# Performance work log

Measured on AMD Instinct MI355X. Metric: run time of the kernel, lower is better.

Reference implementation:

```python
import jax, jax.numpy as jnp
import numpy as np


def _qkernel(r, i, j, k):
    # Build the real-valued block kernel of a quaternion dense layer.
    # r,i,j,k: [in/4, out/4] -> kernel [in, out] implementing the Hamilton product.
    col_r = jnp.concatenate([r, -i, -j, -k], axis=0)
    col_i = jnp.concatenate([i, r, -k, j], axis=0)
    col_j = jnp.concatenate([j, k, r, -i], axis=0)
    col_k = jnp.concatenate([k, -j, i, r], axis=0)
    return jnp.concatenate([col_r, col_i, col_j, col_k], axis=1)


def setup_inputs() -> dict:
    key = jax.random.key(0)
    ks = jax.random.split(key, 12)
    B, F, H = 32768, 1024, 256
    F4, H4 = F // 4, H // 4
    s_in = 1.0 / np.sqrt(F)
    s_h = 1.0 / np.sqrt(H)
    inp = {
        "x": jax.random.normal(ks[0], (B, F), dtype=jnp.float32),
        "wx_r": jax.random.normal(ks[1], (4, F4, H4), dtype=jnp.float32) * s_in,
        "wx_i": jax.random.normal(ks[2], (4, F4, H4), dtype=jnp.float32) * s_in,
        "wx_j": jax.random.normal(ks[3], (4, F4, H4), dtype=jnp.float32) * s_in,
        "wx_k": jax.random.normal(ks[4], (4, F4, H4), dtype=jnp.float32) * s_in,
        "bx": jnp.zeros((4, H), dtype=jnp.float32),
        "uh_r": jax.random.normal(ks[5], (4, H4, H4), dtype=jnp.float32) * s_h,
        "uh_i": jax.random.normal(ks[6], (4, H4, H4), dtype=jnp.float32) * s_h,
        "uh_j": jax.random.normal(ks[7], (4, H4, H4), dtype=jnp.float32) * s_h,
        "uh_k": jax.random.normal(ks[8], (4, H4, H4), dtype=jnp.float32) * s_h,
        "fco_w": jax.random.normal(ks[9], (H, H), dtype=jnp.float32) * s_h,
        "fco_b": jnp.zeros((H,), dtype=jnp.float32),
    }
    return inp


def reference(x, wx_r, wx_i, wx_j, wx_k, bx, uh_r, uh_i, uh_j, uh_k, fco_w, fco_b):
    # Single-step quaternion LSTM cell with zero initial hidden/cell state.
    # Gate order along leading axis: [forget, input, output, cell].
    Kx = jax.vmap(_qkernel)(wx_r, wx_i, wx_j, wx_k)   # [4, F, H]
    Ku = jax.vmap(_qkernel)(uh_r, uh_i, uh_j, uh_k)   # [4, H, H]
    H = bx.shape[1]
    h0 = jnp.zeros((x.shape[0], H), dtype=x.dtype)
    c0 = h0
    gx = jnp.einsum('bf,gfh->gbh', x, Kx) + bx[:, None, :]   # [4, B, H]
    gu = jnp.einsum('bh,ghk->gbk', h0, Ku)                    # [4, B, H]
    z = gx + gu
    ft = jax.nn.sigmoid(z[0])
    it = jax.nn.sigmoid(z[1])
    ot = jax.nn.sigmoid(z[2])
    at = z[3]
    c = it * jnp.tanh(at) + ft * c0
    h = ot * jnp.tanh(c)
    return h @ fco_w + fco_b
```

## Files before the change

kernel.cpp:

```cpp
#include <hip/hip_runtime.h>
#include <cstdint>
#include <cstddef>

#define WS_WP   0
#define WS_FCO  1572864
#define WS_BP   1703936
#define WS_HVP  1707008

typedef __attribute__((ext_vector_type(8))) __bf16 bf16x8;
typedef __attribute__((ext_vector_type(4))) __bf16 bf16x4;
typedef __attribute__((ext_vector_type(4))) float floatx4;

__device__ __forceinline__ unsigned short f2bf(float f) {
  unsigned int u = __builtin_bit_cast(unsigned int, f);
  u += 0x7fffu + ((u >> 16) & 1u);
  return (unsigned short)(u >> 16);
}

__device__ __forceinline__ float sigmf(float z) {
  return __builtin_amdgcn_rcpf(1.f + __expf(-z));
}
__device__ __forceinline__ float tanh_(float z) {
  return 1.f - 2.f * __builtin_amdgcn_rcpf(1.f + __expf(2.f * z));
}

__device__ __forceinline__ void gld16(const void* g, void* l) {
  __builtin_amdgcn_global_load_lds(
      (const __attribute__((address_space(1))) unsigned int*)g,
      (__attribute__((address_space(3))) unsigned int*)l, 16, 0, 0);
}

__global__ __launch_bounds__(256) void pack_k(
    const float* __restrict__ wr, const float* __restrict__ wi,
    const float* __restrict__ wj, const float* __restrict__ wk,
    const float* __restrict__ bx, const float* __restrict__ fw,
    unsigned short* __restrict__ Wp, unsigned short* __restrict__ Fp,
    float* __restrict__ bp) {
  int t = threadIdx.x;
  if (blockIdx.x < 384) {
    int gpp = blockIdx.x >> 7;
    int oct = blockIdx.x & 127;
    int gp = gpp + 1;
    int h = t;
    int hb = h >> 6, hr = h & 63;
    int f0 = oct << 3;
    int fb = f0 >> 8, fr0 = f0 & 255;
    const int   comp_t[4][4] = {{0,1,2,3},{1,0,3,2},{2,3,0,1},{3,2,1,0}};
    const float sign_t[4][4] = {{1.f,-1.f,-1.f,-1.f},{1.f,1.f,-1.f,1.f},
                                {1.f,1.f,1.f,-1.f},{1.f,-1.f,1.f,1.f}};
    const float* srcs[4] = {wr, wi, wj, wk};
    const float* s = srcs[comp_t[hb][fb]] + ((size_t)((gp << 8) + fr0)) * 64 + hr;
    float sg = sign_t[hb][fb];
    unsigned short v[8];
#pragma unroll
    for (int j = 0; j < 8; ++j) v[j] = f2bf(sg * s[(size_t)j * 64]);
    int c = h * 3 + gpp;
    int cb = c / 192, nl = c % 192;
    int kb = oct >> 2, q = oct & 3;
    int idx16 = (nl << 2) + (q ^ ((nl >> 1) & 3));
    uint4 val = make_uint4(
        (unsigned)v[0] | ((unsigned)v[1] << 16), (unsigned)v[2] | ((unsigned)v[3] << 16),
        (unsigned)v[4] | ((unsigned)v[5] << 16), (unsigned)v[6] | ((unsigned)v[7] << 16));
    *(uint4*)(Wp + (size_t)(cb * 32 + kb) * 6144 + idx16 * 8) = val;
    if (oct == 0) bp[c] = bx[(gp << 8) + h];
  } else {
    int oct = blockIdx.x - 384;
    int n = t;
    int k0 = oct << 3;
    unsigned short v[8];
#pragma unroll
    for (int j = 0; j < 8; ++j) v[j] = f2bf(fw[(size_t)(k0 + j) * 256 + n]);
    int nb = n >> 7, nl = n & 127, kb = oct >> 2, q = oct & 3;
    int idx16 = (nl << 2) + (q ^ ((nl >> 1) & 3));
    uint4 val = make_uint4(
        (unsigned)v[0] | ((unsigned)v[1] << 16), (unsigned)v[2] | ((unsigned)v[3] << 16),
        (unsigned)v[4] | ((unsigned)v[5] << 16), (unsigned)v[6] | ((unsigned)v[7] << 16));
    *(uint4*)(Fp + (size_t)((nb << 3) + kb) * 4096 + idx16 * 8) = val;
  }
}

__global__ __launch_bounds__(256, 2) void gemm1_k(
    const float* __restrict__ x, const unsigned short* __restrict__ Wp,
    const float* __restrict__ bp, unsigned short* __restrict__ hvp) {
  __shared__ char smem[40960];
  float* zep = (float*)smem;

  const int t = threadIdx.x;
  const int lane = t & 63, wid = t >> 6;
  const int wm = wid >> 1, wn = wid & 1;
  const int lrow = lane & 15, q = lane >> 4;
  const int rowt = blockIdx.x;
  const int cby = blockIdx.y;
  const int row0 = rowt * 128;
  const float* xbase = x + (size_t)row0 * 1024;
  const unsigned short* wpb = Wp + (size_t)cby * 32 * 6144;

  const int sr = t >> 3, skq = t & 7;
  const int sq8 = skq >> 1, shalf = skq & 1;

  floatx4 acc[4][6];
#pragma unroll
  for (int i = 0; i < 4; ++i)
#pragma unroll
    for (int j = 0; j < 6; ++j) acc[i][j] = (floatx4){0.f, 0.f, 0.f, 0.f};

#define STAGE_B(buf, kt)                                                      \
  {                                                                           \
    unsigned short* sBs_ = (unsigned short*)(smem + (buf) * 20480 + 8192);    \
    const unsigned short* bt_ = wpb + (size_t)(kt) * 6144;                    \
    _Pragma("unroll")                                                         \
    for (int i_ = 0; i_ < 3; ++i_) {                                          \
      int s_ = t + i_ * 256;                                                  \
      gld16(bt_ + s_ * 8, sBs_ + s_ * 8);                                     \
    }                                                                         \
  }
#define LOAD_A(ra, kt)                                                        \
  {                                                                           \
    const float* ab_ = xbase + (kt) * 32 + skq * 4;                           \
    _Pragma("unroll")                                                         \
    for (int i_ = 0; i_ < 4; ++i_)                                            \
      ra[i_] = *(const float4*)(ab_ + (size_t)(i_ * 32 + sr) * 1024);         \
  }
#define WRITE_A(ra, buf)                                                      \
  {                                                                           \
    unsigned short* sAs_ = (unsigned short*)(smem + (buf) * 20480);           \
    _Pragma("unroll")                                                         \
    for (int i_ = 0; i_ < 4; ++i_) {                                          \
      int m_ = i_ * 32 + sr;                                                  \
      int slot_ = (m_ << 2) + (sq8 ^ ((m_ >> 1) & 3));                        \
      bf16x4 v_;                                                              \
      v_[0] = (__bf16)ra[i_].x; v_[1] = (__bf16)ra[i_].y;                     \
      v_[2] = (__bf16)ra[i_].z; v_[3] = (__bf16)ra[i_].w;                     \
      *(bf16x4*)(sAs_ + slot_ * 8 + shalf * 4) = v_;                          \
    }                                                                         \
  }

  {
    float4 r0[4];
    LOAD_A(r0, 0)
    STAGE_B(0, 0)
    WRITE_A(r0, 0)
  }
  float4 ra[4];
  for (int kt = 0; kt < 32; ++kt) {
    __syncthreads();
    if (kt < 31) {
      LOAD_A(ra, kt + 1)
      STAGE_B((kt + 1) & 1, kt + 1)
    }
    const unsigned short* sA = (const unsigned short*)(smem + (kt & 1) * 20480);
    const unsigned short* sB = sA + 4096;
    bf16x8 af[4], bf[6];
#pragma unroll
    for (int mt = 0; mt < 4; ++mt) {
      int m = wm * 64 + mt * 16 + lrow;
      int slot = (m << 2) + (q ^ ((m >> 1) & 3));
      af[mt] = *(const bf16x8*)(const void*)(sA + slot * 8);
    }
#pragma unroll
    for (int nt = 0; nt < 6; ++nt) {
      int n = wn * 96 + nt * 16 + lrow;
      int off16 = (n << 2) + (q ^ ((n >> 1) & 3));
      bf[nt] = *(const bf16x8*)(const void*)(sB + off16 * 8);
    }
#pragma unroll
    for (int mt = 0; mt < 4; ++mt)
#pragma unroll
      for (int nt = 0; nt < 6; ++nt)
        acc[mt][nt] = __builtin_amdgcn_mfma_f32_16x16x32_bf16(af[mt], bf[nt], acc[mt][nt], 0, 0, 0);
    if (kt < 31) WRITE_A(ra, (kt + 1) & 1)
  }
#undef STAGE_B
#undef LOAD_A
#undef WRITE_A
  __syncthreads();

  const float* bp0 = bp + cby * 192;
  const int er = t >> 3, oc = t & 7;
#pragma unroll
  for (int pass = 0; pass < 4; ++pass) {
    if (wm == (pass >> 1)) {
      int mtb = (pass & 1) * 2;
#pragma unroll
      for (int mi = 0; mi < 2; ++mi)
#pragma unroll
        for (int nt = 0; nt < 6; ++nt)
#pragma unroll
          for (int r = 0; r < 4; ++r)
            zep[(mi * 16 + q * 4 + r) * 201 + wn * 96 + nt * 16 + lrow] = acc[mtb + mi][nt][r];
    }
    __syncthreads();
    {
      int ml = pass * 32 + er;
      unsigned short v[8];
#pragma unroll
      for (int j = 0; j < 8; ++j) {
        int hl = oc * 8 + j;
        float zi = zep[er * 201 + hl * 3 + 0] + bp0[hl * 3 + 0];
        float zo = zep[er * 201 + hl * 3 + 1] + bp0[hl * 3 + 1];
        float zc = zep[er * 201 + hl * 3 + 2] + bp0[hl * 3 + 2];
        float it = sigmf(zi);
        float ot = sigmf(zo);
        float cc = it * tanh_(zc);
        v[j] = f2bf(ot * tanh_(cc));
      }
      int ktile = cby * 2 + (oc >> 2), qq = oc & 3;
      int idx16 = (ml << 2) + (qq ^ ((ml >> 1) & 3));
      uint4 val = make_uint4(
          (unsigned)v[0] | ((unsigned)v[1] << 16), (unsigned)v[2] | ((unsigned)v[3] << 16),
          (unsigned)v[4] | ((unsigned)v[5] << 16), (unsigned)v[6] | ((unsigned)v[7] << 16));
      *(uint4*)(hvp + (size_t)(rowt * 8 + ktile) * 4096 + idx16 * 8) = val;
    }
    __syncthreads();
  }
}

__global__ __launch_bounds__(256, 4) void gemm2_k(
    const unsigned short* __restrict__ hvp, const unsigned short* __restrict__ Fp,
    const float* __restrict__ fcob, float* __restrict__ out) {
  __shared__ unsigned short sB[32768];
  const int t = threadIdx.x;
  const int lane = t & 63, wid = t >> 6;
  const int wm = wid >> 1, wn = wid & 1;
  const int lrow = lane & 15, q = lane >> 4;
  const int mb = blockIdx.x, nb = blockIdx.y;

  const unsigned short* fpb = Fp + (size_t)nb * 32768;
#pragma unroll
  for (int i = 0; i < 16; ++i) gld16(fpb + (t + i * 256) * 8, sB + (t + i * 256) * 8);

  floatx4 acc[4][4];
#pragma unroll
  for (int i = 0; i < 4; ++i)
#pragma unroll
    for (int j = 0; j < 4; ++j) acc[i][j] = (floatx4){0.f, 0.f, 0.f, 0.f};
  __syncthreads();

#pragma unroll
  for (int kt = 0; kt < 8; ++kt) {
    const unsigned short* at_ = hvp + (size_t)(mb * 8 + kt) * 4096;
    bf16x8 af[4], bf[4];
#pragma unroll
    for (int mt = 0; mt < 4; ++mt) {
      int m = wm * 64 + mt * 16 + lrow;
      int o = (m << 2) + (q ^ ((m >> 1) & 3));
      af[mt] = *(const bf16x8*)(const void*)(at_ + o * 8);
    }
#pragma unroll
    for (int nt = 0; nt < 4; ++nt) {
      int n = wn * 64 + nt * 16 + lrow;
      int o = (n << 2) + (q ^ ((n >> 1) & 3));
      bf[nt] = *(const bf16x8*)(const void*)(sB + kt * 4096 + o * 8);
    }
#pragma unroll
    for (int mt = 0; mt < 4; ++mt)
#pragma unroll
      for (int nt = 0; nt < 4; ++nt)
        acc[mt][nt] = __builtin_amdgcn_mfma_f32_16x16x32_bf16(af[mt], bf[nt], acc[mt][nt], 0, 0, 0);
  }
#pragma unroll
  for (int nt = 0; nt < 4; ++nt) {
    int colg = nb * 128 + wn * 64 + nt * 16 + lrow;
    float bias = fcob[colg];
#pragma unroll
    for (int mt = 0; mt < 4; ++mt) {
      int rowg = mb * 128 + wm * 64 + mt * 16 + q * 4;
#pragma unroll
      for (int r = 0; r < 4; ++r)
        out[(size_t)(rowg + r) * 256 + colg] = acc[mt][nt][r] + bias;
    }
  }
}

extern "C" void kernel_launch(void* const* d_in, const int* in_sizes, int n_in,
                              void* d_out, int out_size, void* d_ws, size_t ws_size,
                              hipStream_t stream) {
  const float* x  = (const float*)d_in[0];
  const float* wr = (const float*)d_in[1];
  const float* wi = (const float*)d_in[2];
  const float* wj = (const float*)d_in[3];
  const float* wk = (const float*)d_in[4];
  const float* bx = (const float*)d_in[5];
  const float* fw = (const float*)d_in[10];
  const float* fb = (const float*)d_in[11];
  char* ws = (char*)d_ws;
  unsigned short* Wp  = (unsigned short*)(ws + WS_WP);
  unsigned short* Fp  = (unsigned short*)(ws + WS_FCO);
  float*          bp  = (float*)(ws + WS_BP);
  unsigned short* hvp = (unsigned short*)(ws + WS_HVP);
  float*          out = (float*)d_out;

  hipLaunchKernelGGL(pack_k,  dim3(416),    dim3(256), 0, stream, wr, wi, wj, wk, bx, fw, Wp, Fp, bp);
  hipLaunchKernelGGL(gemm1_k, dim3(256, 4), dim3(256), 0, stream, x, Wp, bp, hvp);
  hipLaunchKernelGGL(gemm2_k, dim3(256, 2), dim3(256), 0, stream, hvp, Fp, fb, out);
}
```

Before: 328.0 us.

## Triple-buffer gemm1 shared memory with two-stage-ahead prefetch and explicit waitcnts

Expands the gemm1 K-loop from double to triple buffering in LDS, prefetching the A tile and B stage two iterations ahead with two register sets for the A tiles. __syncthreads is replaced by manual s_waitcnt vmcnt/lgkmcnt and a raw s_barrier, so more global-load latency can overlap the MFMA work. In exchange, LDS per block grows to 60KB and the extra A registers add pressure, which may cut occupancy below the two blocks per CU requested by the launch bounds. The hand-counted vmcnt values are fragile if the compiler emits a different number of loads.

Result: faster. 287.8 us, median of 2 (-12.3%).

```diff
diff --git a/kernel.cpp b/kernel.cpp
--- a/kernel.cpp
+++ b/kernel.cpp
@@ -82,7 +82,7 @@
 __global__ __launch_bounds__(256, 2) void gemm1_k(
     const float* __restrict__ x, const unsigned short* __restrict__ Wp,
     const float* __restrict__ bp, unsigned short* __restrict__ hvp) {
-  __shared__ char smem[40960];
+  __shared__ char smem[61440];
   float* zep = (float*)smem;
 
   const int t = threadIdx.x;
@@ -104,9 +104,9 @@
 #pragma unroll
     for (int j = 0; j < 6; ++j) acc[i][j] = (floatx4){0.f, 0.f, 0.f, 0.f};
 
-#define STAGE_B(buf, kt)                                                      \
-  {                                                                           \
-    unsigned short* sBs_ = (unsigned short*)(smem + (buf) * 20480 + 8192);    \
+#define STAGE_B(bufi, kt)                                                     \
+  {                                                                           \
+    unsigned short* sBs_ = (unsigned short*)(smem + (bufi) * 20480 + 8192);   \
     const unsigned short* bt_ = wpb + (size_t)(kt) * 6144;                    \
     _Pragma("unroll")                                                         \
     for (int i_ = 0; i_ < 3; ++i_) {                                          \
@@ -121,9 +121,9 @@
     for (int i_ = 0; i_ < 4; ++i_)                                            \
       ra[i_] = *(const float4*)(ab_ + (size_t)(i_ * 32 + sr) * 1024);         \
   }
-#define WRITE_A(ra, buf)                                                      \
-  {                                                                           \
-    unsigned short* sAs_ = (unsigned short*)(smem + (buf) * 20480);           \
+#define WRITE_A(ra, bufi)                                                     \
+  {                                                                           \
+    unsigned short* sAs_ = (unsigned short*)(smem + (bufi) * 20480);          \
     _Pragma("unroll")                                                         \
     for (int i_ = 0; i_ < 4; ++i_) {                                          \
       int m_ = i_ * 32 + sr;                                                  \
@@ -134,42 +134,65 @@
       *(bf16x4*)(sAs_ + slot_ * 8 + shalf * 4) = v_;                          \
     }                                                                         \
   }
-
-  {
-    float4 r0[4];
-    LOAD_A(r0, 0)
-    STAGE_B(0, 0)
-    WRITE_A(r0, 0)
-  }
-  float4 ra[4];
-  for (int kt = 0; kt < 32; ++kt) {
-    __syncthreads();
-    if (kt < 31) {
-      LOAD_A(ra, kt + 1)
-      STAGE_B((kt + 1) & 1, kt + 1)
-    }
-    const unsigned short* sA = (const unsigned short*)(smem + (kt & 1) * 20480);
-    const unsigned short* sB = sA + 4096;
-    bf16x8 af[4], bf[6];
-#pragma unroll
-    for (int mt = 0; mt < 4; ++mt) {
-      int m = wm * 64 + mt * 16 + lrow;
-      int slot = (m << 2) + (q ^ ((m >> 1) & 3));
-      af[mt] = *(const bf16x8*)(const void*)(sA + slot * 8);
-    }
-#pragma unroll
-    for (int nt = 0; nt < 6; ++nt) {
-      int n = wn * 96 + nt * 16 + lrow;
-      int off16 = (n << 2) + (q ^ ((n >> 1) & 3));
-      bf[nt] = *(const bf16x8*)(const void*)(sB + off16 * 8);
-    }
-#pragma unroll
-    for (int mt = 0; mt < 4; ++mt)
-#pragma unroll
-      for (int nt = 0; nt < 6; ++nt)
-        acc[mt][nt] = __builtin_amdgcn_mfma_f32_16x16x32_bf16(af[mt], bf[nt], acc[mt][nt], 0, 0, 0);
-    if (kt < 31) WRITE_A(ra, (kt + 1) & 1)
-  }
+#define COMPUTE(bufi)                                                         \
+  {                                                                           \
+    const unsigned short* sA_ = (const unsigned short*)(smem + (bufi) * 20480);\
+    const unsigned short* sB_ = sA_ + 4096;                                   \
+    bf16x8 af[4], bf[6];                                                      \
+    _Pragma("unroll")                                                         \
+    for (int mt = 0; mt < 4; ++mt) {                                          \
+      int m = wm * 64 + mt * 16 + lrow;                                       \
+      int slot = (m << 2) + (q ^ ((m >> 1) & 3));                             \
+      af[mt] = *(const bf16x8*)(const void*)(sA_ + slot * 8);                 \
+    }                                                                         \
+    _Pragma("unroll")                                                         \
+    for (int nt = 0; nt < 6; ++nt) {                                          \
+      int n = wn * 96 + nt * 16 + lrow;                                       \
+      int off16 = (n << 2) + (q ^ ((n >> 1) & 3));                            \
+      bf[nt] = *(const bf16x8*)(const void*)(sB_ + off16 * 8);                \
+    }                                                                         \
+    _Pragma("unroll")                                                         \
+    for (int mt = 0; mt < 4; ++mt)                                            \
+      _Pragma("unroll")                                                       \
+      for (int nt = 0; nt < 6; ++nt)                                          \
+        acc[mt][nt] = __builtin_amdgcn_mfma_f32_16x16x32_bf16(                \
+            af[mt], bf[nt], acc[mt][nt], 0, 0, 0);                            \
+  }
+#define BODY(kt, RC, RN)                                                      \
+  {                                                                           \
+    if ((kt) < 30) {                                                          \
+      LOAD_A(RN, (kt) + 2)                                                    \
+      STAGE_B(((kt) + 2) % 3, (kt) + 2)                                       \
+    }                                                                         \
+    COMPUTE((kt) % 3)                                                         \
+    if ((kt) < 30) {                                                          \
+      asm volatile("s_waitcnt vmcnt(7)" ::: "memory");                        \
+    } else {                                                                  \
+      asm volatile("s_waitcnt vmcnt(0)" ::: "memory");                        \
+    }                                                                         \
+    if ((kt) < 31) { WRITE_A(RC, ((kt) + 1) % 3) }                            \
+    asm volatile("s_waitcnt lgkmcnt(0)" ::: "memory");                        \
+    __builtin_amdgcn_s_barrier();                                             \
+    asm volatile("" ::: "memory");                                            \
+  }
+
+  float4 raA[4], raB[4];
+  LOAD_A(raA, 0)
+  STAGE_B(0, 0)
+  LOAD_A(raB, 1)
+  STAGE_B(1, 1)
+  WRITE_A(raA, 0)
+  asm volatile("s_waitcnt vmcnt(7)" ::: "memory");
+  asm volatile("s_waitcnt lgkmcnt(0)" ::: "memory");
+  __builtin_amdgcn_s_barrier();
+  asm volatile("" ::: "memory");
+
+  for (int kt2 = 0; kt2 < 32; kt2 += 2) {
+    BODY(kt2, raB, raA)
+    BODY(kt2 + 1, raA, raB)
+  }
+#undef BODY
+#undef COMPUTE
 #undef STAGE_B
 #undef LOAD_A
 #undef WRITE_A
```
